# Performance work log

Hardware: AMD Instinct MI355X
Metric: run time of the kernel (lower is better)

Reference implementation:

```python
import jax, jax.numpy as jnp
import numpy as np

EPS = 1e-5
ALPHA = 32.0


def setup_inputs() -> dict:
    key = jax.random.key(0)
    k1, k2 = jax.random.split(key)
    M, D, K = 131072, 256, 512
    x = jax.random.normal(k1, (M, D), dtype=jnp.float32)
    ln_weight = jnp.ones((D,), dtype=jnp.float32)
    ln_bias = jnp.zeros((D,), dtype=jnp.float32)
    cluster_center = jax.random.uniform(k2, (K, D), dtype=jnp.float32)
    return {"x": x, "ln_weight": ln_weight, "ln_bias": ln_bias,
            "cluster_center": cluster_center}


def reference(x, ln_weight, ln_bias, cluster_center):
    # CustomLayerNorm: (x - mean) / (std + eps) * w + b  (std unbiased=False,
    # NOTE eps is added to std, not variance, matching the torch module)
    mean = x.mean(axis=-1, keepdims=True)
    std = jnp.sqrt(((x - mean) ** 2).mean(axis=-1, keepdims=True))
    xn = (x - mean) / (std + EPS) * ln_weight + ln_bias

    # Euclidean cdist via sum-of-squares + GEMM, then sqrt (as in source)
    x_sq = (xn * xn).sum(axis=-1, keepdims=True)            # (M, 1)
    c_sq = (cluster_center * cluster_center).sum(axis=-1)   # (K,)
    d2 = x_sq + c_sq[None, :] - 2.0 * (xn @ cluster_center.T)
    x_distance = jnp.sqrt(d2)                               # (M, K)

    # NegSoftAssign: exp(-alpha * d / mean_d), normalized over last dim
    d_mean = x_distance.mean(axis=-1, keepdims=True)
    logits = -ALPHA * (x_distance / d_mean)
    x_distance_assign = jax.nn.softmax(logits, axis=-1)     # (M, K)

    x_rec = x_distance_assign @ cluster_center              # (M, D)
    return (x_distance, x_distance_assign, x_rec)
```

## Files before the change

kernel.cpp:

```cpp
#include <hip/hip_runtime.h>
#include <hip/hip_bf16.h>
#include <cstdint>

#define M_ROWS 131072
#define D_DIM  256
#define K_CL   512

typedef __attribute__((ext_vector_type(4))) float  f4;
typedef __attribute__((ext_vector_type(8))) short  bfrag;
typedef __attribute__((ext_vector_type(4))) float  ffrag;

#define MFMA16(A,B,C) __builtin_amdgcn_mfma_f32_16x16x32_bf16((A),(B),(C),0,0,0)

__device__ __forceinline__ ffrag fzero() {
    ffrag z;
    z[0] = 0.f; z[1] = 0.f; z[2] = 0.f; z[3] = 0.f;
    return z;
}

__device__ __forceinline__ unsigned short f2bf(float f) {
    unsigned int u = __float_as_uint(f);
    u += 0x7FFFu + ((u >> 16) & 1u);
    return (unsigned short)(u >> 16);
}
__device__ __forceinline__ float bf2f(unsigned short u) {
    return __uint_as_float(((unsigned int)u) << 16);
}

__global__ void prep_kernel(const float* __restrict__ C,
                            unsigned short* __restrict__ Cb,
                            unsigned short* __restrict__ Ct,
                            float* __restrict__ csq)
{
    __shared__ unsigned short lds[64 * 264];
    const int tid = threadIdx.x;
    const int kb  = blockIdx.x * 64;
    const int r   = tid >> 2;
    const int q   = tid & 3;

    const float* cr = C + (size_t)(kb + r) * D_DIM;
    float s = 0.f;
    #pragma unroll
    for (int i = 0; i < 16; ++i) {
        const int j = q * 16 + i;
        f4 v = *(const f4*)(cr + j * 4);
        unsigned short u0 = f2bf(v[0]), u1 = f2bf(v[1]), u2 = f2bf(v[2]), u3 = f2bf(v[3]);
        *(ushort4*)(Cb + (size_t)(kb + r) * D_DIM + j * 4) = make_ushort4(u0, u1, u2, u3);
        *(ushort4*)(lds + r * 264 + j * 4)                  = make_ushort4(u0, u1, u2, u3);
        float f0 = bf2f(u0), f1 = bf2f(u1), f2_ = bf2f(u2), f3 = bf2f(u3);
        s += f0 * f0 + f1 * f1 + f2_ * f2_ + f3 * f3;
    }
    s += __shfl_xor(s, 1, 64);
    s += __shfl_xor(s, 2, 64);
    if (q == 0) csq[kb + r] = s;
    __syncthreads();

    #pragma unroll
    for (int c = 0; c < 16; ++c) {
        ushort4 p = make_ushort4(lds[(c * 4 + 0) * 264 + tid],
                                 lds[(c * 4 + 1) * 264 + tid],
                                 lds[(c * 4 + 2) * 264 + tid],
                                 lds[(c * 4 + 3) * 264 + tid]);
        *(ushort4*)(Ct + (size_t)tid * K_CL + kb + c * 4) = p;
    }
}

__global__ __launch_bounds__(256)
void fused_kernel(const float* __restrict__ x,
                  const float* __restrict__ lnw,
                  const float* __restrict__ lnb,
                  const unsigned short* __restrict__ Cb,
                  const unsigned short* __restrict__ Ct,
                  const float* __restrict__ csq,
                  float* __restrict__ out0,
                  float* __restrict__ out1,
                  float* __restrict__ out2)
{
    __shared__ __align__(16) char smem[34432];
    unsigned short* xn_s = (unsigned short*)smem;
    unsigned short* as_s = (unsigned short*)smem;
    float* red_a = (float*)(smem + 33280);
    float* red_b = (float*)(smem + 33792);
    float* xsq_s = (float*)(smem + 34304);

    const int tid = threadIdx.x;
    const int w   = tid >> 6;
    const int l   = tid & 63;
    const int g   = l >> 4;
    const int cl  = l & 15;
    const int m0  = blockIdx.x * 32;
    const int nb  = w * 128;
    const int db  = w * 64;

    {
        const int rr = tid >> 3, sub = tid & 7;
        const float* xr = x + (size_t)(m0 + rr) * D_DIM;
        f4 xv[8];
        float sum = 0.f, ss = 0.f;
        #pragma unroll
        for (int i = 0; i < 8; ++i) {
            xv[i] = *(const f4*)(xr + (i * 8 + sub) * 4);
            #pragma unroll
            for (int c = 0; c < 4; ++c) { float v = xv[i][c]; sum += v; ss += v * v; }
        }
        #pragma unroll
        for (int msk = 1; msk < 8; msk <<= 1) {
            sum += __shfl_xor(sum, msk, 64);
            ss  += __shfl_xor(ss,  msk, 64);
        }
        const float mean = sum * (1.0f / 256.0f);
        float var = ss * (1.0f / 256.0f) - mean * mean;
        var = fmaxf(var, 0.0f);
        const float inv = 1.0f / (sqrtf(var) + 1e-5f);

        float xsq = 0.f;
        #pragma unroll
        for (int i = 0; i < 8; ++i) {
            f4 wv = *(const f4*)(lnw + (i * 8 + sub) * 4);
            f4 bv = *(const f4*)(lnb + (i * 8 + sub) * 4);
            float a0 = (xv[i][0] - mean) * inv * wv[0] + bv[0];
            float a1 = (xv[i][1] - mean) * inv * wv[1] + bv[1];
            float a2 = (xv[i][2] - mean) * inv * wv[2] + bv[2];
            float a3 = (xv[i][3] - mean) * inv * wv[3] + bv[3];
            unsigned short u0 = f2bf(a0), u1 = f2bf(a1), u2 = f2bf(a2), u3 = f2bf(a3);
            float c0 = bf2f(u0), c1 = bf2f(u1), c2 = bf2f(u2), c3 = bf2f(u3);
            xsq += c0 * c0 + c1 * c1 + c2 * c2 + c3 * c3;
            *(ushort4*)(xn_s + rr * 264 + (i * 8 + sub) * 4) = make_ushort4(u0, u1, u2, u3);
        }
        #pragma unroll
        for (int msk = 1; msk < 8; msk <<= 1) xsq += __shfl_xor(xsq, msk, 64);
        if (sub == 0) xsq_s[rr] = xsq;
    }
    __syncthreads();

    ffrag acc[2][8];
    #pragma unroll
    for (int rt = 0; rt < 2; ++rt)
        #pragma unroll
        for (int nt = 0; nt < 8; ++nt) acc[rt][nt] = fzero();
    {
        bfrag cb[2][4];
        #pragma unroll
        for (int i = 0; i < 4; ++i)
            cb[0][i] = *(const bfrag*)(Cb + (nb + cl) * D_DIM + i * 32 + g * 8);
        #pragma unroll
        for (int bi = 0; bi < 16; ++bi) {
            const int nt = bi >> 1, kh = bi & 1;
            if (bi < 15) {
                const int nn = (bi + 1) >> 1, nk = (bi + 1) & 1;
                #pragma unroll
                for (int i = 0; i < 4; ++i)
                    cb[(bi + 1) & 1][i] = *(const bfrag*)
                        (Cb + (nb + nn * 16 + cl) * D_DIM + (nk * 4 + i) * 32 + g * 8);
            }
            #pragma unroll
            for (int rt = 0; rt < 2; ++rt)
                #pragma unroll
                for (int i = 0; i < 4; ++i) {
                    bfrag xf = *(const bfrag*)
                        (xn_s + (rt * 16 + cl) * 264 + (kh * 4 + i) * 32 + g * 8);
                    acc[rt][nt] = MFMA16(cb[bi & 1][i], xf, acc[rt][nt]);
                }
        }
    }

    float dsum[2];
    dsum[0] = 0.f; dsum[1] = 0.f;
    {
        const float xsqv0 = xsq_s[cl];
        const float xsqv1 = xsq_s[16 + cl];
        #pragma unroll
        for (int nt = 0; nt < 8; ++nt) {
            f4 cs = *(const f4*)(csq + nb + nt * 16 + g * 4);
            #pragma unroll
            for (int rt = 0; rt < 2; ++rt) {
                const float xsqv = rt ? xsqv1 : xsqv0;
                f4 dv;
                #pragma unroll
                for (int r = 0; r < 4; ++r) {
                    float d2 = xsqv + cs[r] - 2.0f * acc[rt][nt][r];
                    dv[r] = sqrtf(fmaxf(d2, 0.0f));
                    acc[rt][nt][r] = dv[r];
                }
                *(f4*)(out0 + (size_t)(m0 + rt * 16 + cl) * K_CL + nb + nt * 16 + g * 4) = dv;
                dsum[rt] += dv[0] + dv[1] + dv[2] + dv[3];
            }
        }
    }
    #pragma unroll
    for (int rt = 0; rt < 2; ++rt) {
        dsum[rt] += __shfl_xor(dsum[rt], 16, 64);
        dsum[rt] += __shfl_xor(dsum[rt], 32, 64);
    }
    if (l < 16) {
        red_a[w * 16 + cl]      = dsum[0];
        red_a[64 + w * 16 + cl] = dsum[1];
    }
    __syncthreads();

    float sc[2];
    #pragma unroll
    for (int rt = 0; rt < 2; ++rt) {
        float t = red_a[rt * 64 + cl] + red_a[rt * 64 + 16 + cl]
                + red_a[rt * 64 + 32 + cl] + red_a[rt * 64 + 48 + cl];
        sc[rt] = 16384.0f / t;
    }

    float es[2];
    #pragma unroll
    for (int rt = 0; rt < 2; ++rt) {
        es[rt] = 0.f;
        #pragma unroll
        for (int nt = 0; nt < 8; ++nt) {
            f4 pv;
            #pragma unroll
            for (int r = 0; r < 4; ++r) {
                float p = __expf(-acc[rt][nt][r] * sc[rt]);
                acc[rt][nt][r] = p;
                pv[r] = p;
                es[rt] += p;
            }
            unsigned int lo = (unsigned int)f2bf(pv[0]) | ((unsigned int)f2bf(pv[1]) << 16);
            unsigned int hi = (unsigned int)f2bf(pv[2]) | ((unsigned int)f2bf(pv[3]) << 16);
            *(uint2*)(as_s + (rt * 16 + cl) * 520 + nb + nt * 16 + g * 4) =
                make_uint2(lo, hi);
        }
        es[rt] += __shfl_xor(es[rt], 16, 64);
        es[rt] += __shfl_xor(es[rt], 32, 64);
    }
    if (l < 16) {
        red_b[w * 16 + cl]      = es[0];
        red_b[64 + w * 16 + cl] = es[1];
    }
    __syncthreads();

    float rn[2];
    #pragma unroll
    for (int rt = 0; rt < 2; ++rt) {
        rn[rt] = 1.0f / (red_b[rt * 64 + cl] + red_b[rt * 64 + 16 + cl]
                       + red_b[rt * 64 + 32 + cl] + red_b[rt * 64 + 48 + cl]);
    }

    #pragma unroll
    for (int rt = 0; rt < 2; ++rt)
        #pragma unroll
        for (int nt = 0; nt < 8; ++nt) {
            f4 av;
            #pragma unroll
            for (int r = 0; r < 4; ++r) av[r] = acc[rt][nt][r] * rn[rt];
            *(f4*)(out1 + (size_t)(m0 + rt * 16 + cl) * K_CL + nb + nt * 16 + g * 4) = av;
        }

    {
        ffrag acc2[2][4];
        #pragma unroll
        for (int rt = 0; rt < 2; ++rt)
            #pragma unroll
            for (int nt = 0; nt < 4; ++nt) acc2[rt][nt] = fzero();

        bfrag ct[2][4];
        #pragma unroll
        for (int i = 0; i < 4; ++i)
            ct[0][i] = *(const bfrag*)(Ct + (db + cl) * K_CL + i * 32 + g * 8);
        #pragma unroll
        for (int bi = 0; bi < 16; ++bi) {
            const int nt = bi >> 2, kb = bi & 3;
            if (bi < 15) {
                const int nn = (bi + 1) >> 2, nk = (bi + 1) & 3;
                #pragma unroll
                for (int i = 0; i < 4; ++i)
                    ct[(bi + 1) & 1][i] = *(const bfrag*)
                        (Ct + (db + nn * 16 + cl) * K_CL + (nk * 4 + i) * 32 + g * 8);
            }
            #pragma unroll
            for (int rt = 0; rt < 2; ++rt)
                #pragma unroll
                for (int i = 0; i < 4; ++i) {
                    bfrag af = *(const bfrag*)
                        (as_s + (rt * 16 + cl) * 520 + (kb * 4 + i) * 32 + g * 8);
                    acc2[rt][nt] = MFMA16(ct[bi & 1][i], af, acc2[rt][nt]);
                }
        }

        #pragma unroll
        for (int rt = 0; rt < 2; ++rt)
            #pragma unroll
            for (int nt = 0; nt < 4; ++nt) {
                f4 rv;
                #pragma unroll
                for (int r = 0; r < 4; ++r) rv[r] = acc2[rt][nt][r] * rn[rt];
                *(f4*)(out2 + (size_t)(m0 + rt * 16 + cl) * D_DIM + db + nt * 16 + g * 4) = rv;
            }
    }
}

extern "C" void kernel_launch(void* const* d_in, const int* in_sizes, int n_in,
                              void* d_out, int out_size, void* d_ws, size_t ws_size,
                              hipStream_t stream)
{
    const float* x   = (const float*)d_in[0];
    const float* lnw = (const float*)d_in[1];
    const float* lnb = (const float*)d_in[2];
    const float* C   = (const float*)d_in[3];

    float* out0 = (float*)d_out;
    float* out1 = out0 + (size_t)M_ROWS * K_CL;
    float* out2 = out1 + (size_t)M_ROWS * K_CL;

    unsigned short* Cb = (unsigned short*)d_ws;
    unsigned short* Ct = Cb + (size_t)K_CL * D_DIM;
    float*          cs = (float*)((char*)d_ws + 2u * K_CL * D_DIM * 2u);

    prep_kernel<<<8, 256, 0, stream>>>(C, Cb, Ct, cs);
    fused_kernel<<<M_ROWS / 32, 256, 0, stream>>>(x, lnw, lnb, Cb, Ct, cs,
                                                  out0, out1, out2);
}
```

Baseline: 342.6 us.

## Interleave epilogue stores with MFMA loops and prefetch cluster fragments earlier

Restructures both GEMM phases into explicitly software-pipelined, macro-unrolled stages. Distance computation and out0 stores now run per N-tile right after that tile's MFMAs, and the out1 stores are spread across the second GEMM's iterations. Cluster-center fragments are prefetched earlier: the first tile before the LayerNorm stage and the Ct tiles before the softmax barrier. The aim is to overlap global stores and loads with matrix work and hide load latency, at the cost of more live registers (two 8-fragment buffers), which may lower occupancy.

```diff
diff --git a/kernel.cpp b/kernel.cpp
--- a/kernel.cpp
+++ b/kernel.cpp
@@ -92,6 +92,66 @@
     const int nb  = w * 128;
     const int db  = w * 64;
 
+#define LOADCB(BUF, NT) {                                                       \
+    const unsigned short* bp_ = Cb + (nb + (NT) * 16 + cl) * D_DIM + g * 8;     \
+    _Pragma("unroll")                                                           \
+    for (int i_ = 0; i_ < 8; ++i_) (BUF)[i_] = *(const bfrag*)(bp_ + i_ * 32); }
+
+#define G1COMP(CUR, NT) {                                                       \
+    ffrag a0_ = fzero(), a1_ = fzero();                                         \
+    _Pragma("unroll")                                                           \
+    for (int i_ = 0; i_ < 8; ++i_) {                                            \
+        bfrag x0_ = *(const bfrag*)(xn_s + cl * 264 + i_ * 32 + g * 8);         \
+        bfrag x1_ = *(const bfrag*)(xn_s + (16 + cl) * 264 + i_ * 32 + g * 8);  \
+        a0_ = MFMA16((CUR)[i_], x0_, a0_);                                      \
+        a1_ = MFMA16((CUR)[i_], x1_, a1_);                                      \
+    }                                                                           \
+    f4 cs_ = *(const f4*)(csq + nb + (NT) * 16 + g * 4);                        \
+    f4 d0_, d1_;                                                                \
+    _Pragma("unroll")                                                           \
+    for (int r_ = 0; r_ < 4; ++r_) {                                            \
+        d0_[r_] = sqrtf(fmaxf(xsqv0 + cs_[r_] - 2.0f * a0_[r_], 0.0f));         \
+        d1_[r_] = sqrtf(fmaxf(xsqv1 + cs_[r_] - 2.0f * a1_[r_], 0.0f));         \
+    }                                                                           \
+    *(f4*)(out0 + (size_t)(m0 + cl) * K_CL + nb + (NT) * 16 + g * 4) = d0_;     \
+    *(f4*)(out0 + (size_t)(m0 + 16 + cl) * K_CL + nb + (NT) * 16 + g * 4) = d1_;\
+    dsum0 += d0_[0] + d0_[1] + d0_[2] + d0_[3];                                 \
+    dsum1 += d1_[0] + d1_[1] + d1_[2] + d1_[3];                                 \
+    acc[0][NT] = d0_;                                                           \
+    acc[1][NT] = d1_; }
+
+#define LOADCT(BUF, BI) {                                                       \
+    const unsigned short* tp_ = Ct + (db + ((BI) >> 2) * 16 + cl) * K_CL        \
+                                + ((BI) & 3) * 128 + g * 8;                     \
+    _Pragma("unroll")                                                           \
+    for (int i_ = 0; i_ < 4; ++i_) (BUF)[i_] = *(const bfrag*)(tp_ + i_ * 32); }
+
+#define G2COMP(CUR, BI) {                                                       \
+    _Pragma("unroll")                                                           \
+    for (int i_ = 0; i_ < 4; ++i_) {                                            \
+        bfrag p0_ = *(const bfrag*)(as_s + cl * 520 + ((BI) & 3) * 128 + i_ * 32 + g * 8); \
+        bfrag p1_ = *(const bfrag*)(as_s + (16 + cl) * 520 + ((BI) & 3) * 128 + i_ * 32 + g * 8); \
+        acc2[0][(BI) >> 2] = MFMA16((CUR)[i_], p0_, acc2[0][(BI) >> 2]);        \
+        acc2[1][(BI) >> 2] = MFMA16((CUR)[i_], p1_, acc2[1][(BI) >> 2]);        \
+    }                                                                           \
+    {   f4 av_;                                                                 \
+        _Pragma("unroll")                                                       \
+        for (int r_ = 0; r_ < 4; ++r_)                                          \
+            av_[r_] = acc[(BI) >> 3][(BI) & 7][r_] * rn[(BI) >> 3];             \
+        *(f4*)(out1 + (size_t)(m0 + ((BI) >> 3) * 16 + cl) * K_CL               \
+               + nb + ((BI) & 7) * 16 + g * 4) = av_; } }
+
+#define G2TILE(NT) {                                                            \
+    _Pragma("unroll")                                                           \
+    for (int rt_ = 0; rt_ < 2; ++rt_) {                                         \
+        f4 rv_;                                                                 \
+        _Pragma("unroll")                                                       \
+        for (int r_ = 0; r_ < 4; ++r_) rv_[r_] = acc2[rt_][NT][r_] * rn[rt_];   \
+        *(f4*)(out2 + (size_t)(m0 + rt_ * 16 + cl) * D_DIM + db + (NT) * 16 + g * 4) = rv_; } }
+
+    bfrag cbA[8], cbB[8];
+    LOADCB(cbA, 0);
+
     {
         const int rr = tid >> 3, sub = tid & 7;
         const float* xr = x + (size_t)(m0 + rr) * D_DIM;
@@ -133,68 +193,28 @@
     }
     __syncthreads();
 
+    const float xsqv0 = xsq_s[cl];
+    const float xsqv1 = xsq_s[16 + cl];
+    float dsum0 = 0.f, dsum1 = 0.f;
     ffrag acc[2][8];
-    #pragma unroll
-    for (int rt = 0; rt < 2; ++rt)
-        #pragma unroll
-        for (int nt = 0; nt < 8; ++nt) acc[rt][nt] = fzero();
-    {
-        bfrag cb[2][4];
-        #pragma unroll
-        for (int i = 0; i < 4; ++i)
-            cb[0][i] = *(const bfrag*)(Cb + (nb + cl) * D_DIM + i * 32 + g * 8);
-        #pragma unroll
-        for (int bi = 0; bi < 16; ++bi) {
-            const int nt = bi >> 1, kh = bi & 1;
-            if (bi < 15) {
-                const int nn = (bi + 1) >> 1, nk = (bi + 1) & 1;
-                #pragma unroll
-                for (int i = 0; i < 4; ++i)
-                    cb[(bi + 1) & 1][i] = *(const bfrag*)
-                        (Cb + (nb + nn * 16 + cl) * D_DIM + (nk * 4 + i) * 32 + g * 8);
-            }
-            #pragma unroll
-            for (int rt = 0; rt < 2; ++rt)
-                #pragma unroll
-                for (int i = 0; i < 4; ++i) {
-                    bfrag xf = *(const bfrag*)
-                        (xn_s + (rt * 16 + cl) * 264 + (kh * 4 + i) * 32 + g * 8);
-                    acc[rt][nt] = MFMA16(cb[bi & 1][i], xf, acc[rt][nt]);
-                }
-        }
-    }
-
-    float dsum[2];
-    dsum[0] = 0.f; dsum[1] = 0.f;
-    {
-        const float xsqv0 = xsq_s[cl];
-        const float xsqv1 = xsq_s[16 + cl];
-        #pragma unroll
-        for (int nt = 0; nt < 8; ++nt) {
-            f4 cs = *(const f4*)(csq + nb + nt * 16 + g * 4);
-            #pragma unroll
-            for (int rt = 0; rt < 2; ++rt) {
-                const float xsqv = rt ? xsqv1 : xsqv0;
-                f4 dv;
-                #pragma unroll
-                for (int r = 0; r < 4; ++r) {
-                    float d2 = xsqv + cs[r] - 2.0f * acc[rt][nt][r];
-                    dv[r] = sqrtf(fmaxf(d2, 0.0f));
-                    acc[rt][nt][r] = dv[r];
-                }
-                *(f4*)(out0 + (size_t)(m0 + rt * 16 + cl) * K_CL + nb + nt * 16 + g * 4) = dv;
-                dsum[rt] += dv[0] + dv[1] + dv[2] + dv[3];
-            }
-        }
-    }
-    #pragma unroll
-    for (int rt = 0; rt < 2; ++rt) {
-        dsum[rt] += __shfl_xor(dsum[rt], 16, 64);
-        dsum[rt] += __shfl_xor(dsum[rt], 32, 64);
-    }
+
+    LOADCB(cbB, 1);
+    G1COMP(cbA, 0); LOADCB(cbA, 2);
+    G1COMP(cbB, 1); LOADCB(cbB, 3);
+    G1COMP(cbA, 2); LOADCB(cbA, 4);
+    G1COMP(cbB, 3); LOADCB(cbB, 5);
+    G1COMP(cbA, 4); LOADCB(cbA, 6);
+    G1COMP(cbB, 5); LOADCB(cbB, 7);
+    G1COMP(cbA, 6);
+    G1COMP(cbB, 7);
+
+    dsum0 += __shfl_xor(dsum0, 16, 64);
+    dsum0 += __shfl_xor(dsum0, 32, 64);
+    dsum1 += __shfl_xor(dsum1, 16, 64);
+    dsum1 += __shfl_xor(dsum1, 32, 64);
     if (l < 16) {
-        red_a[w * 16 + cl]      = dsum[0];
-        red_a[64 + w * 16 + cl] = dsum[1];
+        red_a[w * 16 + cl]      = dsum0;
+        red_a[64 + w * 16 + cl] = dsum1;
     }
     __syncthreads();
 
@@ -205,6 +225,9 @@
                 + red_a[rt * 64 + 32 + cl] + red_a[rt * 64 + 48 + cl];
         sc[rt] = 16384.0f / t;
     }
+
+    bfrag ctA[4], ctB[4];
+    LOADCT(ctA, 0);
 
     float es[2];
     #pragma unroll
@@ -232,6 +255,7 @@
         red_b[w * 16 + cl]      = es[0];
         red_b[64 + w * 16 + cl] = es[1];
     }
+    LOADCT(ctB, 1);
     __syncthreads();
 
     float rn[2];
@@ -241,16 +265,6 @@
                        + red_b[rt * 64 + 32 + cl] + red_b[rt * 64 + 48 + cl]);
     }
 
-    #pragma unroll
-    for (int rt = 0; rt < 2; ++rt)
-        #pragma unroll
-        for (int nt = 0; nt < 8; ++nt) {
-            f4 av;
-            #pragma unroll
-            for (int r = 0; r < 4; ++r) av[r] = acc[rt][nt][r] * rn[rt];
-            *(f4*)(out1 + (size_t)(m0 + rt * 16 + cl) * K_CL + nb + nt * 16 + g * 4) = av;
-        }
-
     {
         ffrag acc2[2][4];
         #pragma unroll
@@ -258,40 +272,29 @@
             #pragma unroll
             for (int nt = 0; nt < 4; ++nt) acc2[rt][nt] = fzero();
 
-        bfrag ct[2][4];
-        #pragma unroll
-        for (int i = 0; i < 4; ++i)
-            ct[0][i] = *(const bfrag*)(Ct + (db + cl) * K_CL + i * 32 + g * 8);
-        #pragma unroll
-        for (int bi = 0; bi < 16; ++bi) {
-            const int nt = bi >> 2, kb = bi & 3;
-            if (bi < 15) {
-                const int nn = (bi + 1) >> 2, nk = (bi + 1) & 3;
-                #pragma unroll
-                for (int i = 0; i < 4; ++i)
-                    ct[(bi + 1) & 1][i] = *(const bfrag*)
-                        (Ct + (db + nn * 16 + cl) * K_CL + (nk * 4 + i) * 32 + g * 8);
-            }
-            #pragma unroll
-            for (int rt = 0; rt < 2; ++rt)
-                #pragma unroll
-                for (int i = 0; i < 4; ++i) {
-                    bfrag af = *(const bfrag*)
-                        (as_s + (rt * 16 + cl) * 520 + (kb * 4 + i) * 32 + g * 8);
-                    acc2[rt][nt] = MFMA16(ct[bi & 1][i], af, acc2[rt][nt]);
-                }
-        }
-
-        #pragma unroll
-        for (int rt = 0; rt < 2; ++rt)
-            #pragma unroll
-            for (int nt = 0; nt < 4; ++nt) {
-                f4 rv;
-                #pragma unroll
-                for (int r = 0; r < 4; ++r) rv[r] = acc2[rt][nt][r] * rn[rt];
-                *(f4*)(out2 + (size_t)(m0 + rt * 16 + cl) * D_DIM + db + nt * 16 + g * 4) = rv;
-            }
-    }
+        G2COMP(ctA, 0);  LOADCT(ctA, 2);
+        G2COMP(ctB, 1);  LOADCT(ctB, 3);
+        G2COMP(ctA, 2);  LOADCT(ctA, 4);
+        G2COMP(ctB, 3);  G2TILE(0); LOADCT(ctB, 5);
+        G2COMP(ctA, 4);  LOADCT(ctA, 6);
+        G2COMP(ctB, 5);  LOADCT(ctB, 7);
+        G2COMP(ctA, 6);  LOADCT(ctA, 8);
+        G2COMP(ctB, 7);  G2TILE(1); LOADCT(ctB, 9);
+        G2COMP(ctA, 8);  LOADCT(ctA, 10);
+        G2COMP(ctB, 9);  LOADCT(ctB, 11);
+        G2COMP(ctA, 10); LOADCT(ctA, 12);
+        G2COMP(ctB, 11); G2TILE(2); LOADCT(ctB, 13);
+        G2COMP(ctA, 12); LOADCT(ctA, 14);
+        G2COMP(ctB, 13); LOADCT(ctB, 15);
+        G2COMP(ctA, 14);
+        G2COMP(ctB, 15); G2TILE(3);
+    }
+
+#undef LOADCB
+#undef G1COMP
+#undef LOADCT
+#undef G2COMP
+#undef G2TILE
 }
 
 extern "C" void kernel_launch(void* const* d_in, const int* in_sizes, int n_in,
```

After: 364.7 us. 1.06x slower.
